# Kernel optimization log

Measured on AMD Instinct MI355X. Metric: run time of the kernel, lower is better.

## Reference

```python
import jax, jax.numpy as jnp
import numpy as np


def setup_inputs() -> dict:
    key = jax.random.key(0)
    k1, k2, k3 = jax.random.split(key, 3)
    N, K, C, M = 16, 32768, 16, 128
    pred_boxes = jax.random.normal(k1, (N, K, 5), dtype=jnp.float32)
    pred_cls = jax.random.normal(k2, (N, K, C), dtype=jnp.float32)
    target = jax.random.uniform(k3, (N, M, 5), dtype=jnp.float32)
    return {"pred_boxes": pred_boxes, "pred_cls": pred_cls, "target": target}


def _losses(pred_boxes, pred_cls, target):
    N, K, _ = pred_boxes.shape
    M = target.shape[1]
    C = pred_cls.shape[2]
    mask = target.sum(axis=2) != 0                      # (N, M)
    maskf = mask.astype(pred_boxes.dtype)
    denom = maskf.sum()
    tboxes = target[..., 1:]                            # (N, M, 4) corners (x1,y1,x2,y2)
    tcls = target[..., 0].astype(jnp.int32)             # (N, M)
    pconf = pred_boxes[..., 4]                          # (N, K)
    pb = pred_boxes[..., :4]                            # (N, K, 4) (x, y, w, h)

    # pred corners (N, 1, K)
    p_x1 = pb[:, None, :, 0]
    p_y1 = pb[:, None, :, 1]
    p_x2 = (pb[..., 2] + pb[..., 0])[:, None, :]
    p_y2 = (pb[..., 3] + pb[..., 1])[:, None, :]
    # target corners (N, M, 1)
    t_x1 = tboxes[..., 0:1]
    t_y1 = tboxes[..., 1:2]
    t_x2 = tboxes[..., 2:3]
    t_y2 = tboxes[..., 3:4]

    ix1 = jnp.maximum(p_x1, t_x1)
    iy1 = jnp.maximum(p_y1, t_y1)
    ix2 = jnp.minimum(p_x2, t_x2)
    iy2 = jnp.minimum(p_y2, t_y2)
    inter = jnp.clip(ix2 - ix1 + 1, 0) * jnp.clip(iy2 - iy1 + 1, 0)   # (N, M, K)
    a1 = (p_x2 - p_x1 + 1) * (p_y2 - p_y1 + 1)
    a2 = (t_x2 - t_x1 + 1) * (t_y2 - t_y1 + 1)
    iou = inter / (a1 + a2 - inter + 1e-16)

    best = jnp.argmax(iou, axis=-1)                     # (N, M)
    best_idx = jnp.where(mask, best, 0)                 # masked targets keep index 0 (as torch init)

    best_pb = jnp.take_along_axis(pb, best_idx[..., None], axis=1)       # (N, M, 4)
    best_cls = jnp.take_along_axis(pred_cls, best_idx[..., None], axis=1)  # (N, M, C)
    # NOTE: faithful to original: conf gather indices are never updated -> always index 0
    conf_idx = jnp.zeros((N, M), dtype=jnp.int32)
    best_conf = jax.nn.sigmoid(jnp.take_along_axis(pconf, conf_idx, axis=1))  # (N, M)

    def masked_mean(v):
        return (v * maskf).sum() / denom

    logp = jax.nn.log_softmax(best_cls, axis=-1)
    ce = -jnp.take_along_axis(logp, tcls[..., None], axis=-1)[..., 0]
    loss_cls = masked_mean(ce)

    loss_x = masked_mean((best_pb[..., 0] - tboxes[..., 0]) ** 2)
    loss_y = masked_mean((best_pb[..., 1] - tboxes[..., 1]) ** 2)
    loss_w = masked_mean((best_pb[..., 2] - (tboxes[..., 2] - tboxes[..., 0])) ** 2)
    loss_h = masked_mean((best_pb[..., 3] - (tboxes[..., 3] - tboxes[..., 1])) ** 2)

    labels = (best_conf > 0.5).astype(best_conf.dtype)
    bce = -(labels * jnp.log(best_conf) + (1.0 - labels) * jnp.log(1.0 - best_conf))
    loss_conf = masked_mean(bce)

    loss = loss_cls + loss_x + loss_y + loss_w + loss_h + loss_conf
    return loss, loss_cls, loss_x, loss_y, loss_w, loss_h, loss_conf


def reference(pred_boxes, pred_cls, target):
    return _losses(pred_boxes, pred_cls, target)
```

## Files before the change

### kernel.cpp

```cpp
#include <hip/hip_runtime.h>
#include <math.h>

constexpr int N_ = 16;
constexpr int K_ = 32768;
constexpr int C_ = 16;
constexpr int M_ = 128;

constexpr int KC = 512;
constexpr int CPB = 2;
constexpr int CPW = K_ / (KC * CPB);
constexpr int WAVES = 8;

#define POISON_U 0xAAAAAAAAu

__device__ __forceinline__ unsigned long long load_agent_u64(
    const unsigned long long* p) {
  return __hip_atomic_load(p, __ATOMIC_RELAXED, __HIP_MEMORY_SCOPE_AGENT);
}
__device__ __forceinline__ void store_agent_u64(unsigned long long* p,
                                                unsigned long long v) {
  __hip_atomic_store(p, v, __ATOMIC_RELAXED, __HIP_MEMORY_SCOPE_AGENT);
}
__device__ __forceinline__ void store_agent_f32(float* p, float v) {
  __hip_atomic_store(p, v, __ATOMIC_RELAXED, __HIP_MEMORY_SCOPE_AGENT);
}
__device__ __forceinline__ float load_agent_f32(const float* p) {
  return __hip_atomic_load(p, __ATOMIC_RELAXED, __HIP_MEMORY_SCOPE_AGENT);
}

__device__ __forceinline__ float vminf_(float a, float b) {
  float r;
  asm("v_min_f32 %0, %1, %2" : "=v"(r) : "v"(a), "v"(b));
  return r;
}
__device__ __forceinline__ float vmaxf_(float a, float b) {
  float r;
  asm("v_max_f32 %0, %1, %2" : "=v"(r) : "v"(a), "v"(b));
  return r;
}
__device__ __forceinline__ float vmax0_(float a) {
  float r;
  asm("v_max_f32 %0, 0, %1" : "=v"(r) : "v"(a));
  return r;
}
__device__ __forceinline__ int vbfi_key_(unsigned mask, unsigned iou_bits,
                                         unsigned idx6) {
  int r;
  asm("v_bfi_b32 %0, %1, %2, %3" : "=v"(r) : "v"(mask), "v"(iou_bits),
      "v"(idx6));
  return r;
}

__global__ __launch_bounds__(512, 4) void fused_loss_kernel(
    const float* __restrict__ pred_boxes,
    const float* __restrict__ pred_cls,
    const float* __restrict__ target,
    unsigned long long* __restrict__ rowwin,
    float* __restrict__ ws2,
    int* __restrict__ cnt,
    float* __restrict__ out) {
  __shared__ float4 lds4[KC];
  __shared__ float ldsa1[KC];
  __shared__ int key_s[WAVES][CPB][M_];
  __shared__ float red[WAVES][7];
  __shared__ int s_flag;

  const int bx = blockIdx.x;
  const int n = blockIdx.y;
  const int tid = threadIdx.x;

  const int wv = tid >> 6;
  const int lane = tid & 63;
  const int rb = lane & 31;
  const int half = (lane >> 5) & 1;
  const int ks = (wv * 2 + half) * 32;
  const int hbase = ((1 - half) << 5) | 31;

  float tx1[4], ty1[4], tx2[4], ty2[4], a2[4];
#pragma unroll
  for (int j = 0; j < 4; ++j) {
    const float* tg = target + ((size_t)(n * M_ + rb + 32 * j)) * 5;
    tx1[j] = tg[1];
    ty1[j] = tg[2];
    tx2[j] = tg[3] + 1.0f;
    ty2[j] = tg[4] + 1.0f;
    a2[j] = (tg[3] - tg[1] + 1.0f) * (tg[4] - tg[2] + 1.0f) + 1e-16f;
  }

  const unsigned keymask = 0xFFFFFE00u;

  for (int cc = 0; cc < CPB; ++cc) {
    const int k0 = (bx * CPB + cc) * KC;

    {
      const float* p = pred_boxes + ((size_t)(n * K_ + k0 + tid)) * 5;
      const float x = p[0];
      const float y = p[1];
      const float bw = p[2];
      const float bh = p[3];
      const float px2 = bw + x;
      const float py2 = bh + y;
      lds4[tid] = make_float4(x, y, px2 + 1.0f, py2 + 1.0f);
      ldsa1[tid] = (px2 - x + 1.0f) * (py2 - y + 1.0f);
    }
    __syncthreads();

    int best[4];
#pragma unroll
    for (int j = 0; j < 4; ++j) best[j] = (int)0x80000000;

#pragma unroll 8
    for (int kl = 0; kl < 32; ++kl) {
      const float4 v = lds4[ks + kl];
      const float a1 = ldsa1[ks + kl];
      const unsigned idx6 = (unsigned)(hbase - kl);
#pragma unroll
      for (int j = 0; j < 4; ++j) {
        float ww = vminf_(v.z, tx2[j]) - vmaxf_(v.x, tx1[j]);
        float hh = vminf_(v.w, ty2[j]) - vmaxf_(v.y, ty1[j]);
        ww = vmax0_(ww);
        hh = vmax0_(hh);
        const float inter = ww * hh;
        const float iou = inter * __builtin_amdgcn_rcpf((a1 + a2[j]) - inter);
        const int key = vbfi_key_(keymask, __float_as_uint(iou), idx6);
        best[j] = best[j] > key ? best[j] : key;
      }
    }

#pragma unroll
    for (int j = 0; j < 4; ++j) {
      const int other = __shfl_xor(best[j], 32, 64);
      best[j] = best[j] > other ? best[j] : other;
    }
    if (lane < 32) {
      const unsigned wvf = (unsigned)(7 - wv) << 6;
#pragma unroll
      for (int j = 0; j < 4; ++j) {
        const unsigned u = (unsigned)best[j];
        key_s[wv][cc][rb + 32 * j] = (int)((u & 0xFFFFFE00u) | wvf | (u & 63u));
      }
    }
    __syncthreads();
  }

  if (tid < M_) {
    unsigned long long bestu = ~0ull;
#pragma unroll
    for (int cc = 0; cc < CPB; ++cc) {
      int mg = key_s[0][cc][tid];
#pragma unroll
      for (int w2 = 1; w2 < WAVES; ++w2) {
        const int v = key_s[w2][cc][tid];
        mg = mg > v ? mg : v;
      }
      const unsigned e = (unsigned)mg & 511u;
      const int gk = (bx * CPB + cc) * KC + (511 - (int)e);
      const unsigned tr = (unsigned)mg & 0xFFFFFE00u;
      const unsigned ord = tr ^ (unsigned)(((int)tr >> 31) | 0x80000000);
      const unsigned long long u =
          ((unsigned long long)(~ord) << 32) | (unsigned)gk;
      bestu = u < bestu ? u : bestu;
    }
    store_agent_u64(&rowwin[((size_t)n * CPW + bx) * M_ + tid], bestu);
  }

  __syncthreads();
  if (tid == 0) {
    const unsigned old = (unsigned)atomicAdd(&cnt[n], 1);
    s_flag = (old == POISON_U + (CPW - 1)) || (old == CPW - 1);
  }
  __syncthreads();
  if (!s_flag) return;

  {
    const int m = tid & (M_ - 1);
    float acc[7] = {0, 0, 0, 0, 0, 0, 0};
    if (tid < M_) {
      unsigned long long bestk = ~0ull;
#pragma unroll
      for (int g = 0; g < CPW; ++g) {
        const unsigned long long pk =
            load_agent_u64(&rowwin[((size_t)n * CPW + g) * M_ + m]);
        bestk = pk < bestk ? pk : bestk;
      }
      const int bidx0 = (int)(unsigned)bestk;

      const float* tg2 = target + ((size_t)(n * M_ + m)) * 5;
      const float t0 = tg2[0], t1 = tg2[1], t2 = tg2[2], t3 = tg2[3],
                  t4 = tg2[4];
      const float sum5 = t0 + t1 + t2 + t3 + t4;
      const float mk = (sum5 != 0.0f) ? 1.0f : 0.0f;
      const int bidx = (sum5 != 0.0f) ? bidx0 : 0;

      const float* pb = pred_boxes + ((size_t)(n * K_ + bidx)) * 5;
      const float b0 = pb[0], b1 = pb[1], bw = pb[2], bh = pb[3];

      const float4* pc =
          (const float4*)(pred_cls + ((size_t)(n * K_ + bidx)) * C_);
      float vals[C_];
#pragma unroll
      for (int q = 0; q < 4; ++q) {
        const float4 vv = pc[q];
        vals[q * 4 + 0] = vv.x;
        vals[q * 4 + 1] = vv.y;
        vals[q * 4 + 2] = vv.z;
        vals[q * 4 + 3] = vv.w;
      }
      int tcls = (int)t0;
      tcls = tcls < 0 ? 0 : (tcls >= C_ ? C_ - 1 : tcls);
      float mx = -INFINITY;
#pragma unroll
      for (int q = 0; q < C_; ++q) mx = fmaxf(mx, vals[q]);
      float se = 0.0f;
#pragma unroll
      for (int q = 0; q < C_; ++q) se += expf(vals[q] - mx);
      const float ce2 = logf(se) + mx - vals[tcls];

      const float dx = b0 - t1;
      const float dy = b1 - t2;
      const float dw = bw - (t3 - t1);
      const float dh = bh - (t4 - t2);

      const float pcf = pred_boxes[(size_t)n * K_ * 5 + 4];
      const float bc = 1.0f / (1.0f + expf(-pcf));
      const float bce = (bc > 0.5f) ? -logf(bc) : -logf(1.0f - bc);

      acc[0] = mk;
      acc[1] = mk * ce2;
      acc[2] = mk * dx * dx;
      acc[3] = mk * dy * dy;
      acc[4] = mk * dw * dw;
      acc[5] = mk * dh * dh;
      acc[6] = mk * bce;
    }

#pragma unroll
    for (int i = 0; i < 7; ++i) {
      float v = acc[i];
      for (int off = 32; off > 0; off >>= 1) v += __shfl_down(v, off, 64);
      acc[i] = v;
    }
    const int lane2 = tid & 63;
    const int wid = tid >> 6;
    if (lane2 == 0) {
#pragma unroll
      for (int i = 0; i < 7; ++i) red[wid][i] = acc[i];
    }
    __syncthreads();

    if (tid == 0) {
      float sum7[7];
#pragma unroll
      for (int i = 0; i < 7; ++i) {
        float s = 0.0f;
#pragma unroll
        for (int w2 = 0; w2 < WAVES; ++w2) s += red[w2][i];
        sum7[i] = s;
      }
#pragma unroll
      for (int i = 0; i < 7; ++i) store_agent_f32(&ws2[n * 8 + i], sum7[i]);
    }
    __syncthreads();
    if (tid == 0) {
      const unsigned old2 = (unsigned)atomicAdd(&cnt[N_], 1);
      s_flag = (old2 == POISON_U + (N_ - 1)) || (old2 == N_ - 1);
    }
    __syncthreads();
  }

  if (s_flag && tid == 0) {
    float s[7] = {0, 0, 0, 0, 0, 0, 0};
    for (int nn = 0; nn < N_; ++nn)
#pragma unroll
      for (int i = 0; i < 7; ++i) s[i] += load_agent_f32(&ws2[nn * 8 + i]);
    const float denom = s[0];
    const float lc = s[1] / denom;
    const float lx = s[2] / denom;
    const float ly = s[3] / denom;
    const float lw = s[4] / denom;
    const float lh = s[5] / denom;
    const float lf = s[6] / denom;
    out[0] = lc + lx + ly + lw + lh + lf;
    out[1] = lc;
    out[2] = lx;
    out[3] = ly;
    out[4] = lw;
    out[5] = lh;
    out[6] = lf;
  }
}

extern "C" void kernel_launch(void* const* d_in, const int* in_sizes, int n_in,
                              void* d_out, int out_size, void* d_ws, size_t ws_size,
                              hipStream_t stream) {
  const float* pred_boxes = (const float*)d_in[0];
  const float* pred_cls = (const float*)d_in[1];
  const float* target = (const float*)d_in[2];
  float* out = (float*)d_out;

  unsigned long long* rowwin = (unsigned long long*)d_ws;
  float* ws2 = (float*)(rowwin + (size_t)N_ * CPW * M_);
  int* cnt = (int*)(ws2 + N_ * 8);

  dim3 g(CPW, N_);
  fused_loss_kernel<<<g, 512, 0, stream>>>(pred_boxes, pred_cls, target,
                                           rowwin, ws2, cnt, out);
}
```

Baseline: 112.6 us.

## Prefetch second chunk's pred boxes into registers before the first compute pass

Result: no change. 113.3 us (+0.6%).

```diff
diff --git a/kernel.cpp b/kernel.cpp
--- a/kernel.cpp
+++ b/kernel.cpp
@@ -59,8 +59,8 @@
     float* __restrict__ ws2,
     int* __restrict__ cnt,
     float* __restrict__ out) {
-  __shared__ float4 lds4[KC];
-  __shared__ float ldsa1[KC];
+  __shared__ float4 lds4[CPB][KC];
+  __shared__ float ldsa1[CPB][KC];
   __shared__ int key_s[WAVES][CPB][M_];
   __shared__ float red[WAVES][7];
   __shared__ int s_flag;
@@ -75,6 +75,12 @@
   const int half = (lane >> 5) & 1;
   const int ks = (wv * 2 + half) * 32;
   const int hbase = ((1 - half) << 5) | 31;
+
+  const float* p0 =
+      pred_boxes + ((size_t)(n * K_ + bx * (CPB * KC) + tid)) * 5;
+  const float x0 = p0[0], y0 = p0[1], w0 = p0[2], h0 = p0[3];
+  const float* p1 = p0 + (size_t)KC * 5;
+  float x1 = p1[0], y1 = p1[1], w1 = p1[2], h1 = p1[3];
 
   float tx1[4], ty1[4], tx2[4], ty2[4], a2[4];
 #pragma unroll
@@ -87,61 +93,73 @@
     a2[j] = (tg[3] - tg[1] + 1.0f) * (tg[4] - tg[2] + 1.0f) + 1e-16f;
   }
 
+  {
+    const float px2 = w0 + x0;
+    const float py2 = h0 + y0;
+    lds4[0][tid] = make_float4(x0, y0, px2 + 1.0f, py2 + 1.0f);
+    ldsa1[0][tid] = (px2 - x0 + 1.0f) * (py2 - y0 + 1.0f);
+  }
+  asm volatile("" : "+v"(x1), "+v"(y1), "+v"(w1), "+v"(h1));
+  __syncthreads();
+
   const unsigned keymask = 0xFFFFFE00u;
 
-  for (int cc = 0; cc < CPB; ++cc) {
-    const int k0 = (bx * CPB + cc) * KC;
-
-    {
-      const float* p = pred_boxes + ((size_t)(n * K_ + k0 + tid)) * 5;
-      const float x = p[0];
-      const float y = p[1];
-      const float bw = p[2];
-      const float bh = p[3];
-      const float px2 = bw + x;
-      const float py2 = bh + y;
-      lds4[tid] = make_float4(x, y, px2 + 1.0f, py2 + 1.0f);
-      ldsa1[tid] = (px2 - x + 1.0f) * (py2 - y + 1.0f);
-    }
-    __syncthreads();
-
-    int best[4];
-#pragma unroll
-    for (int j = 0; j < 4; ++j) best[j] = (int)0x80000000;
-
-#pragma unroll 8
-    for (int kl = 0; kl < 32; ++kl) {
-      const float4 v = lds4[ks + kl];
-      const float a1 = ldsa1[ks + kl];
-      const unsigned idx6 = (unsigned)(hbase - kl);
-#pragma unroll
-      for (int j = 0; j < 4; ++j) {
-        float ww = vminf_(v.z, tx2[j]) - vmaxf_(v.x, tx1[j]);
-        float hh = vminf_(v.w, ty2[j]) - vmaxf_(v.y, ty1[j]);
-        ww = vmax0_(ww);
-        hh = vmax0_(hh);
-        const float inter = ww * hh;
-        const float iou = inter * __builtin_amdgcn_rcpf((a1 + a2[j]) - inter);
-        const int key = vbfi_key_(keymask, __float_as_uint(iou), idx6);
-        best[j] = best[j] > key ? best[j] : key;
-      }
-    }
-
-#pragma unroll
-    for (int j = 0; j < 4; ++j) {
-      const int other = __shfl_xor(best[j], 32, 64);
-      best[j] = best[j] > other ? best[j] : other;
-    }
-    if (lane < 32) {
-      const unsigned wvf = (unsigned)(7 - wv) << 6;
-#pragma unroll
-      for (int j = 0; j < 4; ++j) {
-        const unsigned u = (unsigned)best[j];
-        key_s[wv][cc][rb + 32 * j] = (int)((u & 0xFFFFFE00u) | wvf | (u & 63u));
-      }
-    }
-    __syncthreads();
-  }
+#define COMPUTE_PASS(B, BEST)                                              \
+  _Pragma("unroll 8") for (int kl = 0; kl < 32; ++kl) {                    \
+    const float4 v = lds4[B][ks + kl];                                     \
+    const float a1 = ldsa1[B][ks + kl];                                    \
+    const unsigned idx6 = (unsigned)(hbase - kl);                          \
+    _Pragma("unroll") for (int j = 0; j < 4; ++j) {                        \
+      float ww = vminf_(v.z, tx2[j]) - vmaxf_(v.x, tx1[j]);                \
+      float hh = vminf_(v.w, ty2[j]) - vmaxf_(v.y, ty1[j]);                \
+      ww = vmax0_(ww);                                                     \
+      hh = vmax0_(hh);                                                     \
+      const float inter = ww * hh;                                         \
+      const float iou =                                                    \
+          inter * __builtin_amdgcn_rcpf((a1 + a2[j]) - inter);             \
+      const int key = vbfi_key_(keymask, __float_as_uint(iou), idx6);      \
+      BEST[j] = BEST[j] > key ? BEST[j] : key;                             \
+    }                                                                      \
+  }
+
+#define MERGE_PUBLISH(B, BEST)                                             \
+  _Pragma("unroll") for (int j = 0; j < 4; ++j) {                          \
+    const int other = __shfl_xor(BEST[j], 32, 64);                         \
+    BEST[j] = BEST[j] > other ? BEST[j] : other;                           \
+  }                                                                        \
+  if (lane < 32) {                                                         \
+    const unsigned wvf = (unsigned)(7 - wv) << 6;                          \
+    _Pragma("unroll") for (int j = 0; j < 4; ++j) {                        \
+      const unsigned u = (unsigned)BEST[j];                                \
+      key_s[wv][B][rb + 32 * j] =                                          \
+          (int)((u & 0xFFFFFE00u) | wvf | (u & 63u));                      \
+    }                                                                      \
+  }
+
+  {
+    int best0[4];
+#pragma unroll
+    for (int j = 0; j < 4; ++j) best0[j] = (int)0x80000000;
+    COMPUTE_PASS(0, best0)
+    MERGE_PUBLISH(0, best0)
+  }
+
+  {
+    const float px2 = w1 + x1;
+    const float py2 = h1 + y1;
+    lds4[1][tid] = make_float4(x1, y1, px2 + 1.0f, py2 + 1.0f);
+    ldsa1[1][tid] = (px2 - x1 + 1.0f) * (py2 - y1 + 1.0f);
+  }
+  __syncthreads();
+
+  {
+    int best1[4];
+#pragma unroll
+    for (int j = 0; j < 4; ++j) best1[j] = (int)0x80000000;
+    COMPUTE_PASS(1, best1)
+    MERGE_PUBLISH(1, best1)
+  }
+  __syncthreads();
 
   if (tid < M_) {
     unsigned long long bestu = ~0ull;
```
